# Performance work log

Measured on AMD Instinct MI355X. Metric: run time of the kernel, lower is better.

Reference implementation:

```python
import jax, jax.numpy as jnp
import numpy as np

EPS = 1e-06


def setup_inputs() -> dict:
    key = jax.random.key(0)
    ks = jax.random.split(key, 8)
    B, T, D = 4, 1024, 1024  # module requires T == D (diagonal einsum)
    s = 1.0 / np.sqrt(D)
    return {
        "x_seq": jax.random.normal(ks[0], (B, T, D), dtype=jnp.float32),
        "gamma": jnp.asarray(0.9, dtype=jnp.float32),
        "Wq": jax.random.normal(ks[1], (D, D), dtype=jnp.float32) * s,
        "bq": jax.random.normal(ks[2], (D,), dtype=jnp.float32) * 0.01,
        "Wk": jax.random.normal(ks[3], (D, D), dtype=jnp.float32) * s,
        "bk": jax.random.normal(ks[4], (D,), dtype=jnp.float32) * 0.01,
        "Wv": jax.random.normal(ks[5], (D, D), dtype=jnp.float32) * s,
        "bv": jax.random.normal(ks[6], (D,), dtype=jnp.float32) * 0.01,
    }


def reference(x_seq, gamma, Wq, bq, Wk, bk, Wv, bv):
    # Faithful math of SUPRAParallelFixedGamma.forward. Notes on fidelity:
    # - torch einsum 'ij,bjdj->bidj' takes the DIAGONAL of kv over (time, last
    #   v-dim), i.e. kv[b,j,d,j] = k[b,j,d] * v[b,j,j]; requires T == D.
    # - gamma_exponents = arange(T)[None,:] - arange(T)[:,None] -> E[i,j] = max(j-i, 0)
    #   (the clamp leaves PAST entries at gamma**0 == 1 and decays FUTURE ones).
    # - S = cumsum over dim 1 (the 'i'/time-output axis) then contracted with q;
    #   this factors exactly as C = cumsum(G, axis=0) applied as a (T,T) weight,
    #   avoiding the original's O(B*T*D*T) intermediate while computing the same math.
    B, T, D = x_seq.shape
    q = jax.nn.relu(x_seq @ Wq.T + bq)          # phi(W_q x)
    k = jax.nn.relu(x_seq @ Wk.T + bk)          # phi(W_k x)
    v = x_seq @ Wv.T + bv
    t = jnp.arange(T)
    E = jnp.maximum(t[None, :] - t[:, None], 0).astype(x_seq.dtype)  # (T,T)
    G = gamma ** E                               # gamma_powers[i,j] = gamma**max(j-i,0)
    C = jnp.cumsum(G, axis=0)                    # C[t,j] = sum_{t'<=t} G[t',j]
    vd = jnp.diagonal(v, axis1=1, axis2=2)       # (B,T): v[b,j,j]  (T==D)
    kv_diag = k * vd[:, :, None]                 # (B,T,D): kv[b,j,d,j]
    # num[b,t,j] = sum_d q[b,t,d] * C[t,j] * kv_diag[b,j,d]
    num = C[None, :, :] * jnp.einsum('btd,bjd->btj', q, kv_diag)
    # Z[b,t,d] = cumsum_t of (G @ k) = sum_j C[t,j] k[b,j,d]
    Z = jnp.einsum('tj,bjd->btd', C, k)
    denom = jnp.sum(q * Z, axis=-1, keepdims=True) + EPS
    return num / denom
```

## Files before the change

### kernel.cpp

```cpp
#include <hip/hip_runtime.h>

typedef __attribute__((ext_vector_type(8))) short bf16x8;
typedef __attribute__((ext_vector_type(4))) float f32x4;


__device__ __forceinline__ unsigned short f2bf(float f) {
    unsigned int u = __builtin_bit_cast(unsigned int, f);
    u += 0x7fffu + ((u >> 16) & 1u);
    return (unsigned short)(u >> 16);
}

__device__ __forceinline__ float bf2f(unsigned short s) {
    return __builtin_bit_cast(float, (unsigned int)s << 16);
}

__device__ __forceinline__ void g2lds16(const unsigned short* g, unsigned short* l) {
    __builtin_amdgcn_global_load_lds(
        (const __attribute__((address_space(1))) unsigned int*)g,
        (__attribute__((address_space(3))) unsigned int*)l, 16, 0, 0);
}


__global__ __launch_bounds__(256)
void prep_kernel(const float* __restrict__ x, const float* __restrict__ wq,
                 const float* __restrict__ wk, const float* __restrict__ Wv,
                 const float* __restrict__ bv, unsigned short* __restrict__ xb,
                 unsigned short* __restrict__ wqk, float* __restrict__ vd,
                 int M, int n4w) {
    const int tid = threadIdx.x;
    if ((int)blockIdx.x < M) {
        const int row = blockIdx.x;
        const int j = row & 1023;
        const int e4 = row * 256 + tid;
        float4 v = reinterpret_cast<const float4*>(x)[e4];
        union { unsigned short s[4]; uint2 u; } o;
        o.s[0] = f2bf(v.x); o.s[1] = f2bf(v.y); o.s[2] = f2bf(v.z); o.s[3] = f2bf(v.w);
        reinterpret_cast<uint2*>(xb)[e4] = o.u;

        float4 w = reinterpret_cast<const float4*>(Wv + (size_t)j * 1024)[tid];
        float s = v.x * w.x + v.y * w.y + v.z * w.z + v.w * w.w;
        #pragma unroll
        for (int off = 32; off; off >>= 1) s += __shfl_down(s, off, 64);
        __shared__ float red[4];
        if ((tid & 63) == 0) red[tid >> 6] = s;
        __syncthreads();
        if (tid == 0) vd[row] = red[0] + red[1] + red[2] + red[3] + bv[j];
    } else {
        int i = (blockIdx.x - M) * 256 + tid;
        const float* src;
        if (i < n4w) { src = wq; }
        else         { src = wk; }
        float4 v = reinterpret_cast<const float4*>(src)[i - (i < n4w ? 0 : n4w)];
        union { unsigned short s[4]; uint2 u; } o;
        o.s[0] = f2bf(v.x); o.s[1] = f2bf(v.y); o.s[2] = f2bf(v.z); o.s[3] = f2bf(v.w);
        reinterpret_cast<uint2*>(wqk)[i] = o.u;
    }
}


__global__ __launch_bounds__(256, 2)
void gemm_qk_kernel(const unsigned short* __restrict__ A, const unsigned short* __restrict__ Bm,
                    unsigned short* __restrict__ qb, unsigned short* __restrict__ kb,
                    const float* __restrict__ bq, const float* __restrict__ bk, int K) {
    __shared__ unsigned short lA[2][128 * 64];
    __shared__ unsigned short lB[2][128 * 64];

    const int tid = threadIdx.x;
    const int lane = tid & 63;
    const int wid = tid >> 6;
    const int wr = wid >> 1;
    const int wc = wid & 1;
    const int tileM = blockIdx.y * 128, tileN = blockIdx.x * 128;

    const int srow = tid >> 3;
    const int scolL = (tid & 7) * 8;
    const int scolG = ((tid & 7) ^ (srow & 7)) * 8;
    const int frow = lane & 15;
    const int fq = lane >> 4;
    const int fsw = frow & 7;

    f32x4 acc[4][4];
    #pragma unroll
    for (int m = 0; m < 4; ++m)
        #pragma unroll
        for (int n = 0; n < 4; ++n)
            acc[m][n] = (f32x4){0.f, 0.f, 0.f, 0.f};

    auto stage = [&](int buf, int k0) {
        #pragma unroll
        for (int j = 0; j < 4; ++j) {
            int r = j * 32 + srow;
            g2lds16(A + (size_t)(tileM + r) * K + (k0 + scolG),  &lA[buf][r * 64 + scolL]);
            g2lds16(Bm + (size_t)(tileN + r) * K + (k0 + scolG), &lB[buf][r * 64 + scolL]);
        }
    };

    stage(0, 0);
    __syncthreads();
    int cur = 0;
    for (int k0 = 0; k0 < K; k0 += 64) {
        if (k0 + 64 < K) stage(cur ^ 1, k0 + 64);

        #pragma unroll
        for (int kk = 0; kk < 2; ++kk) {
            const int g = ((kk * 4 + fq) ^ fsw) * 8;
            bf16x8 af[4], bfr[4];
            #pragma unroll
            for (int m = 0; m < 4; ++m)
                af[m] = *reinterpret_cast<const bf16x8*>(
                    &lA[cur][(wr * 64 + m * 16 + frow) * 64 + g]);
            #pragma unroll
            for (int n = 0; n < 4; ++n)
                bfr[n] = *reinterpret_cast<const bf16x8*>(
                    &lB[cur][(wc * 64 + n * 16 + frow) * 64 + g]);

            #pragma unroll
            for (int m = 0; m < 4; ++m)
                #pragma unroll
                for (int n = 0; n < 4; ++n)
                    acc[m][n] = __builtin_amdgcn_mfma_f32_16x16x32_bf16(af[m], bfr[n], acc[m][n], 0, 0, 0);
        }

        __syncthreads();
        cur ^= 1;
    }

    const int orow = (lane >> 4) * 4;
    const int ocol = lane & 15;
    const bool isQ = tileN < 1024;
    unsigned short* Cq = isQ ? qb : kb;
    const float* bias = isQ ? bq : bk;
    const int cb = tileN - (isQ ? 0 : 1024);

    #pragma unroll
    for (int n = 0; n < 4; ++n) {
        int col = cb + wc * 64 + n * 16 + ocol;
        float bia = bias[col];
        #pragma unroll
        for (int m = 0; m < 4; ++m) {
            #pragma unroll
            for (int i = 0; i < 4; ++i) {
                int row = tileM + wr * 64 + m * 16 + orow + i;
                float v = acc[m][n][i] + bia;
                Cq[(size_t)row * 1024 + col] = f2bf(v > 0.f ? v : 0.f);
            }
        }
    }
}


__global__ __launch_bounds__(256, 3)
void gemm_attn_kernel(const unsigned short* __restrict__ A, const unsigned short* __restrict__ Bm,
                      unsigned short* __restrict__ nmb, const float* __restrict__ vd,
                      float* __restrict__ dpart, const float* __restrict__ gammap,
                      int K, int Mtot) {
    __shared__ unsigned short lA[2][64 * 32];
    __shared__ unsigned short lB[2][128 * 32];

    const int tid = threadIdx.x;
    const int lane = tid & 63;
    const int wid = tid >> 6;
    const int wr = wid >> 1, wc = wid & 1;
    const int tileM = blockIdx.y * 64, tileN = blockIdx.x * 128;

    const unsigned short* Ab = A + (size_t)blockIdx.z * 1024 * 1024;
    const unsigned short* Bb = Bm + (size_t)blockIdx.z * 1024 * 1024;

    const int r0 = tid >> 2;
    const int r1 = (tid + 256) >> 2;
    const int cc = (tid & 3) * 8;
    const int frow = lane & 15;
    const int fk = (lane >> 4) * 8;

    f32x4 acc[2][4];
    #pragma unroll
    for (int m = 0; m < 2; ++m)
        #pragma unroll
        for (int n = 0; n < 4; ++n)
            acc[m][n] = (f32x4){0.f, 0.f, 0.f, 0.f};

    auto stage = [&](int buf, int k0) {
        g2lds16(Ab + (size_t)(tileM + r0) * K + (k0 + cc), &lA[buf][tid * 8]);
        g2lds16(Bb + (size_t)(tileN + r0) * K + (k0 + cc), &lB[buf][tid * 8]);
        g2lds16(Bb + (size_t)(tileN + r1) * K + (k0 + cc), &lB[buf][2048 + tid * 8]);
    };

    stage(0, 0);
    __syncthreads();
    int cur = 0;
    for (int k0 = 0; k0 < K; k0 += 32) {
        if (k0 + 32 < K) stage(cur ^ 1, k0 + 32);

        bf16x8 af[2], bfr[4];
        #pragma unroll
        for (int m = 0; m < 2; ++m)
            af[m] = *reinterpret_cast<const bf16x8*>(&lA[cur][(wr * 32 + m * 16 + frow) * 32 + fk]);
        #pragma unroll
        for (int n = 0; n < 4; ++n)
            bfr[n] = *reinterpret_cast<const bf16x8*>(&lB[cur][(wc * 64 + n * 16 + frow) * 32 + fk]);

        #pragma unroll
        for (int m = 0; m < 2; ++m)
            #pragma unroll
            for (int n = 0; n < 4; ++n)
                acc[m][n] = __builtin_amdgcn_mfma_f32_16x16x32_bf16(af[m], bfr[n], acc[m][n], 0, 0, 0);

        __syncthreads();
        cur ^= 1;
    }

    const int orow = (lane >> 4) * 4;
    const int ocol = lane & 15;

    unsigned short* ob = nmb + (size_t)blockIdx.z * 1024 * 1024;
    const float* vdb = vd + blockIdx.z * 1024;
    const float g = gammap[0];
    const float l2g = log2f(g);
    const float inv1mg = 1.f / (1.f - g);
    const float c1 = g * inv1mg;

    int jcol[4]; float gj[4], vdv[4];
    #pragma unroll
    for (int n = 0; n < 4; ++n) {
        jcol[n] = tileN + wc * 64 + n * 16 + ocol;
        gj[n] = exp2f((float)jcol[n] * l2g);
        vdv[n] = vdb[jcol[n]];
    }

    #pragma unroll
    for (int m = 0; m < 2; ++m) {
        #pragma unroll
        for (int i = 0; i < 4; ++i) {
            int t = tileM + wr * 32 + m * 16 + orow + i;
            float gt = exp2f((float)t * l2g);
            float ctf = (1.f - g * gt) * inv1mg;
            float s = 0.f;
            #pragma unroll
            for (int n = 0; n < 4; ++n) {
                int j = jcol[n];
                float Cfut = exp2f((float)(j - t) * l2g) * ctf;
                float Cpast = (float)(t - j + 1) + c1 * (1.f - gj[n]);
                float Cw = (j <= t) ? Cpast : Cfut;
                float v = acc[m][n][i];
                s += Cw * v;
                ob[(size_t)t * 1024 + j] = f2bf(Cw * vdv[n] * v);
            }
            s += __shfl_xor(s, 1, 64);
            s += __shfl_xor(s, 2, 64);
            s += __shfl_xor(s, 4, 64);
            s += __shfl_xor(s, 8, 64);
            if ((lane & 15) == 0)
                dpart[(size_t)(blockIdx.x * 2 + wc) * Mtot + blockIdx.z * 1024 + t] = s;
        }
    }
}


__global__ __launch_bounds__(256)
void scale_kernel(const unsigned short* __restrict__ nmb, float* __restrict__ out,
                  const float* __restrict__ dpart, int Mtot) {
    int r = blockIdx.x;
    float s = 1e-6f;
    #pragma unroll
    for (int p = 0; p < 16; ++p) s += dpart[(size_t)p * Mtot + r];
    float inv = 1.f / s;
    const uint2* src = reinterpret_cast<const uint2*>(nmb + (size_t)r * 1024);
    float4* dst = reinterpret_cast<float4*>(out + (size_t)r * 1024);
    uint2 u = src[threadIdx.x];
    float4 v = { bf2f((unsigned short)(u.x & 0xffff)) * inv,
                 bf2f((unsigned short)(u.x >> 16))    * inv,
                 bf2f((unsigned short)(u.y & 0xffff)) * inv,
                 bf2f((unsigned short)(u.y >> 16))    * inv };
    dst[threadIdx.x] = v;
}


extern "C" void kernel_launch(void* const* d_in, const int* in_sizes, int n_in,
                              void* d_out, int out_size, void* d_ws, size_t ws_size,
                              hipStream_t stream) {
    const float* x     = (const float*)d_in[0];
    const float* gamma = (const float*)d_in[1];
    const float* Wq    = (const float*)d_in[2];
    const float* bq    = (const float*)d_in[3];
    const float* Wk    = (const float*)d_in[4];
    const float* bk    = (const float*)d_in[5];
    const float* Wv    = (const float*)d_in[6];
    const float* bv    = (const float*)d_in[7];
    float* out = (float*)d_out;

    const int D = 1024, T = 1024;
    const int B = in_sizes[0] / (T * D);
    const int M = B * T;

    char* ws = (char*)d_ws;
    size_t off = 0;
    unsigned short* xb  = (unsigned short*)(ws + off); off += (size_t)M * D * 2;
    unsigned short* wqk = (unsigned short*)(ws + off); off += (size_t)2 * D * D * 2;
    unsigned short* qb  = (unsigned short*)(ws + off); off += (size_t)M * D * 2;
    unsigned short* kb  = (unsigned short*)(ws + off); off += (size_t)M * D * 2;
    float* vd    = (float*)(ws + off); off += (size_t)M * 4;
    float* dpart = (float*)(ws + off); off += (size_t)16 * M * 4;
    unsigned short* nmb = xb;

    const int n4w = D * D / 4;

    prep_kernel<<<dim3(M + 2 * n4w / 256), 256, 0, stream>>>(
        x, Wq, Wk, Wv, bv, xb, wqk, vd, M, n4w);

    gemm_qk_kernel<<<dim3(2048 / 128, M / 128), 256, 0, stream>>>(
        xb, wqk, qb, kb, bq, bk, D);

    gemm_attn_kernel<<<dim3(T / 128, T / 64, B), 256, 0, stream>>>(
        qb, kb, nmb, vd, dpart, gamma, D, M);

    scale_kernel<<<dim3(M), 256, 0, stream>>>(nmb, out, dpart, M);
}
```

Before: 67.40 us.

## Double K tile to 64 with XOR-swizzled LDS layout in attention GEMM

The attention GEMM now stages 64-wide K slices instead of 32, which halves the number of loop iterations and barriers. The global-to-LDS copy permutes 16-byte chunks by XOR with the row index, and the fragment reads apply the same swizzle, to avoid LDS bank conflicts on the wider rows. LDS use per block doubles, which may limit how many blocks fit on a CU under launch_bounds(256,3).

```diff
diff --git a/kernel.cpp b/kernel.cpp
--- a/kernel.cpp
+++ b/kernel.cpp
@@ -154,8 +154,8 @@
                       unsigned short* __restrict__ nmb, const float* __restrict__ vd,
                       float* __restrict__ dpart, const float* __restrict__ gammap,
                       int K, int Mtot) {
-    __shared__ unsigned short lA[2][64 * 32];
-    __shared__ unsigned short lB[2][128 * 32];
+    __shared__ unsigned short lA[2][64 * 64];
+    __shared__ unsigned short lB[2][128 * 64];
 
     const int tid = threadIdx.x;
     const int lane = tid & 63;
@@ -166,11 +166,12 @@
     const unsigned short* Ab = A + (size_t)blockIdx.z * 1024 * 1024;
     const unsigned short* Bb = Bm + (size_t)blockIdx.z * 1024 * 1024;
 
-    const int r0 = tid >> 2;
-    const int r1 = (tid + 256) >> 2;
-    const int cc = (tid & 3) * 8;
+    const int srow = tid >> 3;
+    const int scolL = (tid & 7) * 8;
+    const int scolG = ((tid & 7) ^ (srow & 7)) * 8;
     const int frow = lane & 15;
-    const int fk = (lane >> 4) * 8;
+    const int fq = lane >> 4;
+    const int fsw = frow & 7;
 
     f32x4 acc[2][4];
     #pragma unroll
@@ -180,30 +181,43 @@
             acc[m][n] = (f32x4){0.f, 0.f, 0.f, 0.f};
 
     auto stage = [&](int buf, int k0) {
-        g2lds16(Ab + (size_t)(tileM + r0) * K + (k0 + cc), &lA[buf][tid * 8]);
-        g2lds16(Bb + (size_t)(tileN + r0) * K + (k0 + cc), &lB[buf][tid * 8]);
-        g2lds16(Bb + (size_t)(tileN + r1) * K + (k0 + cc), &lB[buf][2048 + tid * 8]);
+        #pragma unroll
+        for (int j = 0; j < 2; ++j) {
+            int r = j * 32 + srow;
+            g2lds16(Ab + (size_t)(tileM + r) * K + (k0 + scolG), &lA[buf][r * 64 + scolL]);
+        }
+        #pragma unroll
+        for (int j = 0; j < 4; ++j) {
+            int r = j * 32 + srow;
+            g2lds16(Bb + (size_t)(tileN + r) * K + (k0 + scolG), &lB[buf][r * 64 + scolL]);
+        }
     };
 
     stage(0, 0);
     __syncthreads();
     int cur = 0;
-    for (int k0 = 0; k0 < K; k0 += 32) {
-        if (k0 + 32 < K) stage(cur ^ 1, k0 + 32);
-
-        bf16x8 af[2], bfr[4];
-        #pragma unroll
-        for (int m = 0; m < 2; ++m)
-            af[m] = *reinterpret_cast<const bf16x8*>(&lA[cur][(wr * 32 + m * 16 + frow) * 32 + fk]);
-        #pragma unroll
-        for (int n = 0; n < 4; ++n)
-            bfr[n] = *reinterpret_cast<const bf16x8*>(&lB[cur][(wc * 64 + n * 16 + frow) * 32 + fk]);
-
-        #pragma unroll
-        for (int m = 0; m < 2; ++m)
+    for (int k0 = 0; k0 < K; k0 += 64) {
+        if (k0 + 64 < K) stage(cur ^ 1, k0 + 64);
+
+        #pragma unroll
+        for (int kk = 0; kk < 2; ++kk) {
+            const int g = ((kk * 4 + fq) ^ fsw) * 8;
+            bf16x8 af[2], bfr[4];
+            #pragma unroll
+            for (int m = 0; m < 2; ++m)
+                af[m] = *reinterpret_cast<const bf16x8*>(
+                    &lA[cur][(wr * 32 + m * 16 + frow) * 64 + g]);
             #pragma unroll
             for (int n = 0; n < 4; ++n)
-                acc[m][n] = __builtin_amdgcn_mfma_f32_16x16x32_bf16(af[m], bfr[n], acc[m][n], 0, 0, 0);
+                bfr[n] = *reinterpret_cast<const bf16x8*>(
+                    &lB[cur][(wc * 64 + n * 16 + frow) * 64 + g]);
+
+            #pragma unroll
+            for (int m = 0; m < 2; ++m)
+                #pragma unroll
+                for (int n = 0; n < 4; ++n)
+                    acc[m][n] = __builtin_amdgcn_mfma_f32_16x16x32_bf16(af[m], bfr[n], acc[m][n], 0, 0, 0);
+        }
 
         __syncthreads();
         cur ^= 1;
```

New measurement: 63.81 us (median of 3 runs). -5.3%, faster.
